# Kernel tuning notes

Measured on AMD Instinct MI355X. Metric: run time of the kernel, lower is better.

## Reference

```python
import jax, jax.numpy as jnp
from jax import lax
import numpy as np

B, T, D_IN = 4, 1024, 8
D_MODEL, N_LAYERS, HORIZON, D_OUT = 512, 2, 24, 8
D_STATE, D_CONV, EXPAND = 64, 4, 2
D_INNER = EXPAND * D_MODEL
DT_RANK = -(-D_MODEL // 16)  # ceil(d_model/16) = 32
LN_EPS = 1e-5


def setup_inputs() -> dict:
    key = jax.random.key(0)
    ks = iter(jax.random.split(key, 24))
    rn = lambda shape, s: jax.random.normal(next(ks), shape, jnp.float32) * s
    A_log = jnp.tile(jnp.log(jnp.arange(1, D_STATE + 1, dtype=jnp.float32)), (N_LAYERS, D_INNER, 1))
    return {
        "x": rn((B, T, D_IN), 1.0),
        "W_in": rn((D_IN, D_MODEL), 0.3), "b_in": jnp.zeros((D_MODEL,), jnp.float32),
        "W_xz": rn((N_LAYERS, D_MODEL, 2 * D_INNER), 0.04),
        "conv_w": rn((N_LAYERS, D_INNER, D_CONV), 0.3), "conv_b": jnp.zeros((N_LAYERS, D_INNER), jnp.float32),
        "W_xproj": rn((N_LAYERS, D_INNER, DT_RANK + 2 * D_STATE), 0.03),
        "W_dt": rn((N_LAYERS, DT_RANK, D_INNER), 0.1), "b_dt": rn((N_LAYERS, D_INNER), 0.1) - 4.0,
        "A_log": A_log, "D_skip": jnp.ones((N_LAYERS, D_INNER), jnp.float32),
        "W_out": rn((N_LAYERS, D_INNER, D_MODEL), 0.03),
        "ln_g": jnp.ones((D_MODEL,), jnp.float32), "ln_b": jnp.zeros((D_MODEL,), jnp.float32),
        "W_h1": rn((D_MODEL, D_MODEL), 0.04), "b_h1": jnp.zeros((D_MODEL,), jnp.float32),
        "W_h2": rn((D_MODEL, HORIZON * D_OUT), 0.04), "b_h2": jnp.zeros((HORIZON * D_OUT,), jnp.float32),
    }


def mamba_block(h, Wxz, cw, cb, Wxp, Wdt, bdt, Alog, Dsk, Wout):
    # h: [B,T,d_model] -> [B,T,d_model]  (mamba-ssm Mamba block, no residual)
    xz = h @ Wxz                                   # [B,T,2*d_inner]
    xb, z = jnp.split(xz, 2, axis=-1)
    # depthwise causal conv over time
    xc = jnp.transpose(xb, (0, 2, 1))              # [B,d_inner,T]
    xc = lax.conv_general_dilated(xc, cw[:, None, :], (1,), [(D_CONV - 1, 0)],
                                  feature_group_count=D_INNER)
    xc = jax.nn.silu(xc + cb[None, :, None])
    xc = jnp.transpose(xc, (0, 2, 1))              # [B,T,d_inner]
    # input-dependent dt, B, C
    xdb = xc @ Wxp                                 # [B,T,dt_rank+2*d_state]
    dt_r = xdb[..., :DT_RANK]
    Bc = xdb[..., DT_RANK:DT_RANK + D_STATE]
    Cc = xdb[..., DT_RANK + D_STATE:]
    dt = jax.nn.softplus(dt_r @ Wdt + bdt)         # [B,T,d_inner]
    A = -jnp.exp(Alog)                             # [d_inner,d_state]

    def step(hst, ins):
        dt_t, B_t, C_t, x_t = ins                  # [B,d_inner],[B,N],[B,N],[B,d_inner]
        dA = jnp.exp(dt_t[..., None] * A)          # [B,d_inner,N]
        hst = dA * hst + dt_t[..., None] * B_t[:, None, :] * x_t[..., None]
        y = jnp.einsum('bdn,bn->bd', hst, C_t)
        return hst, y

    h0 = jnp.zeros((h.shape[0], D_INNER, D_STATE), h.dtype)
    xs = (jnp.transpose(dt, (1, 0, 2)), jnp.transpose(Bc, (1, 0, 2)),
          jnp.transpose(Cc, (1, 0, 2)), jnp.transpose(xc, (1, 0, 2)))
    _, ys = lax.scan(step, h0, xs)                 # ys: [T,B,d_inner]
    y = jnp.transpose(ys, (1, 0, 2)) + Dsk * xc
    y = y * jax.nn.silu(z)
    return y @ Wout


def reference(x, W_in, b_in, W_xz, conv_w, conv_b, W_xproj, W_dt, b_dt, A_log, D_skip,
              W_out, ln_g, ln_b, W_h1, b_h1, W_h2, b_h2):
    h = x @ W_in + b_in                            # [B,T,d_model]
    for i in range(N_LAYERS):
        h = mamba_block(h, W_xz[i], conv_w[i], conv_b[i], W_xproj[i], W_dt[i],
                        b_dt[i], A_log[i], D_skip[i], W_out[i])
    mu = jnp.mean(h, axis=-1, keepdims=True)
    var = jnp.mean(jnp.square(h - mu), axis=-1, keepdims=True)
    h = (h - mu) * lax.rsqrt(var + LN_EPS) * ln_g + ln_b
    last = h[:, -1, :]                             # [B,d_model]
    hid = jax.nn.gelu(last @ W_h1 + b_h1, approximate=False)
    yhat = hid @ W_h2 + b_h2                       # [B,horizon*d_out]
    return yhat.reshape(x.shape[0], HORIZON, D_OUT)
```

## Files before the change

### kernel.cpp

```cpp
#include <hip/hip_runtime.h>
#include <hip/hip_bf16.h>

static constexpr int kB      = 4;
static constexpr int kT      = 1024;
static constexpr int kDIN    = 8;
static constexpr int kDMODEL = 512;
static constexpr int kNLAYER = 2;
static constexpr int kHOR    = 24;
static constexpr int kDOUT   = 8;
static constexpr int kDSTATE = 64;
static constexpr int kDINNER = 1024;
static constexpr int kDTRANK = 32;
static constexpr int kXPROJ  = 160;
static constexpr int kXPAD   = 256;
static constexpr int kBT     = kB * kT;

typedef __bf16 bf16x8 __attribute__((ext_vector_type(8)));
typedef float  f32x4  __attribute__((ext_vector_type(4)));

__device__ __forceinline__ float silu_f(float x)     { return x / (1.f + __expf(-x)); }
__device__ __forceinline__ float softplus_f(float x) { return (x > 20.f) ? x : log1pf(__expf(x)); }
__device__ __forceinline__ float gelu_f(float x)     { return 0.5f * x * (1.f + erff(x * 0.70710678118654752f)); }

__device__ __forceinline__ void gld_lds16(const void* g, void* l) {
    __builtin_amdgcn_global_load_lds(
        (const __attribute__((address_space(1))) unsigned int*)g,
        (__attribute__((address_space(3))) unsigned int*)l, 16, 0, 0);
}

template<int CTRL>
__device__ __forceinline__ float dpp_mov(float v) {
    return __int_as_float(__builtin_amdgcn_update_dpp(
        0, __float_as_int(v), CTRL, 0xf, 0xf, false));
}

__global__ __launch_bounds__(256) void wtrans_kernel(
    const float* __restrict__ in, int K, int N, int in_lstride,
    __hip_bfloat16* __restrict__ out, int Kpad, int out_lstride)
{
    __shared__ float tile[32][33];
    const int tid = threadIdx.x;
    const int n0 = blockIdx.x * 32;
    const int k0 = blockIdx.y * 32;
    const float* inl = in + (size_t)blockIdx.z * in_lstride;
    __hip_bfloat16* outl = out + (size_t)blockIdx.z * out_lstride;

#pragma unroll
    for (int p = 0; p < 4; ++p) {
        int idx = p * 256 + tid;
        int ki = idx >> 5, ni = idx & 31;
        float v = 0.f;
        if (k0 + ki < K && n0 + ni < N) v = inl[(size_t)(k0 + ki) * N + n0 + ni];
        tile[ki][ni] = v;
    }
    __syncthreads();
#pragma unroll
    for (int p = 0; p < 4; ++p) {
        int idx = p * 256 + tid;
        int ni = idx >> 5, ki = idx & 31;
        outl[(size_t)(n0 + ni) * Kpad + k0 + ki] = __float2bfloat16(tile[ki][ni]);
    }
}

template<int MODE>
__global__ __launch_bounds__(256) void mfma_gemm_bt(
    const __hip_bfloat16* __restrict__ A, int lda,
    const __hip_bfloat16* __restrict__ BT, int ldb,
    const float* __restrict__ bias,
    float* __restrict__ C, int ldc,
    void* __restrict__ C2,
    int K)
{
    __shared__ __align__(16) __hip_bfloat16 sA[128][64];
    __shared__ __align__(16) __hip_bfloat16 sB[128][64];

    const int tid  = threadIdx.x;
    const int lane = tid & 63;
    const int w    = tid >> 6;
    const int wm   = w >> 1, wn = w & 1;
    const int m0   = blockIdx.y * 128;
    const int n0   = blockIdx.x * 128;

    f32x4 acc[4][4] = {};

    const int lrow = lane & 15;
    const int lk   = (lane >> 4) << 3;

    const int grow = tid >> 3;
    const int gcol = (tid & 7) * 8;
    char* ldsA = (char*)&sA[0][0] + w * 1024;
    char* ldsB = (char*)&sB[0][0] + w * 1024;

    for (int k0 = 0; k0 < K; k0 += 64) {
        __syncthreads();
#pragma unroll
        for (int p = 0; p < 4; ++p) {
            gld_lds16(A  + (size_t)(m0 + grow + p * 32) * lda + k0 + gcol, ldsA + p * 4096);
            gld_lds16(BT + (size_t)(n0 + grow + p * 32) * ldb + k0 + gcol, ldsB + p * 4096);
        }
        __syncthreads();
#pragma unroll
        for (int ks = 0; ks < 2; ++ks) {
            bf16x8 af[4], bfr[4];
#pragma unroll
            for (int i = 0; i < 4; ++i) {
                af[i]  = *reinterpret_cast<const bf16x8*>(&sA[wm * 64 + i * 16 + lrow][ks * 32 + lk]);
                bfr[i] = *reinterpret_cast<const bf16x8*>(&sB[wn * 64 + i * 16 + lrow][ks * 32 + lk]);
            }
#pragma unroll
            for (int i = 0; i < 4; ++i)
#pragma unroll
                for (int j = 0; j < 4; ++j)
                    acc[i][j] = __builtin_amdgcn_mfma_f32_16x16x32_bf16(af[i], bfr[j], acc[i][j], 0, 0, 0);
        }
    }

    const int crow = (lane >> 4) * 4;
    const int ccol = lane & 15;
#pragma unroll
    for (int i = 0; i < 4; ++i) {
#pragma unroll
        for (int j = 0; j < 4; ++j) {
#pragma unroll
            for (int r = 0; r < 4; ++r) {
                int row = m0 + wm * 64 + i * 16 + crow + r;
                int col = n0 + wn * 64 + j * 16 + ccol;
                float v = acc[i][j][r];
                if (MODE == 1) {
                    C[(size_t)row * ldc + col] = v;
                    ((__hip_bfloat16*)C2)[(size_t)row * ldc + col] = __float2bfloat16(v);
                } else if (MODE == 2) {
                    C[(size_t)row * ldc + col] = softplus_f(v + bias[col]);
                } else if (MODE == 4) {
                    if (col < kDINNER)
                        ((__hip_bfloat16*)C)[(size_t)row * ldc + col] = __float2bfloat16(v);
                    else
                        ((__hip_bfloat16*)C2)[(size_t)row * ldc + (col - kDINNER)] =
                            __float2bfloat16(silu_f(v));
                } else {
                    if (col < kDTRANK)
                        ((__hip_bfloat16*)C2)[(size_t)row * kXPAD + col] = __float2bfloat16(v);
                    else if (col < kDTRANK + kDSTATE)
                        C[(size_t)row * 128 + (col - kDTRANK) * 2] = v;
                    else if (col < kXPROJ)
                        C[(size_t)row * 128 + (col - kDTRANK - kDSTATE) * 2 + 1] = v;
                }
            }
        }
    }
}

__global__ __launch_bounds__(256) void in_proj_kernel(
    const float* __restrict__ x, const float* __restrict__ W,
    const float* __restrict__ b,
    float* __restrict__ h, __hip_bfloat16* __restrict__ hb)
{
    int idx = blockIdx.x * 256 + threadIdx.x;
    int n4 = (idx & 127) * 4;
    int m  = idx >> 7;
    float4 acc = *reinterpret_cast<const float4*>(b + n4);
    const float* xr = x + m * kDIN;
#pragma unroll
    for (int k = 0; k < kDIN; ++k) {
        float4 wv = *reinterpret_cast<const float4*>(W + k * kDMODEL + n4);
        float xv = xr[k];
        acc.x = fmaf(xv, wv.x, acc.x);
        acc.y = fmaf(xv, wv.y, acc.y);
        acc.z = fmaf(xv, wv.z, acc.z);
        acc.w = fmaf(xv, wv.w, acc.w);
    }
    *reinterpret_cast<float4*>(h + (size_t)m * kDMODEL + n4) = acc;
    __bf16 o4[4] = {(__bf16)acc.x, (__bf16)acc.y, (__bf16)acc.z, (__bf16)acc.w};
    *reinterpret_cast<ushort4*>(hb + (size_t)m * kDMODEL + n4) =
        *reinterpret_cast<ushort4*>(o4);
}

__global__ __launch_bounds__(256) void conv_silu_kernel(
    const __hip_bfloat16* __restrict__ xb,
    const float* __restrict__ cw, const float* __restrict__ cb,
    __hip_bfloat16* __restrict__ xc)
{
    int idx = blockIdx.x * 256 + threadIdx.x;
    int dg  = (idx & 127) * 8;
    int bt  = idx >> 7;
    int t   = bt & (kT - 1);

    float4 wv[8];
#pragma unroll
    for (int k = 0; k < 8; ++k)
        wv[k] = *reinterpret_cast<const float4*>(cw + (dg + k) * 4);

    float acc[8];
#pragma unroll
    for (int k = 0; k < 8; ++k) acc[k] = cb[dg + k];

    const __hip_bfloat16* base = xb + (size_t)bt * kDINNER + dg;
    {
        bf16x8 v = *reinterpret_cast<const bf16x8*>(base);
#pragma unroll
        for (int k = 0; k < 8; ++k) acc[k] = fmaf((float)v[k], wv[k].w, acc[k]);
    }
    if (t >= 1) {
        bf16x8 v = *reinterpret_cast<const bf16x8*>(base - kDINNER);
#pragma unroll
        for (int k = 0; k < 8; ++k) acc[k] = fmaf((float)v[k], wv[k].z, acc[k]);
    }
    if (t >= 2) {
        bf16x8 v = *reinterpret_cast<const bf16x8*>(base - 2 * kDINNER);
#pragma unroll
        for (int k = 0; k < 8; ++k) acc[k] = fmaf((float)v[k], wv[k].y, acc[k]);
    }
    if (t >= 3) {
        bf16x8 v = *reinterpret_cast<const bf16x8*>(base - 3 * kDINNER);
#pragma unroll
        for (int k = 0; k < 8; ++k) acc[k] = fmaf((float)v[k], wv[k].x, acc[k]);
    }
    bf16x8 o;
#pragma unroll
    for (int k = 0; k < 8; ++k) o[k] = (__bf16)silu_f(acc[k]);
    *reinterpret_cast<bf16x8*>(xc + (size_t)bt * kDINNER + dg) = o;
}

__global__ __launch_bounds__(256, 4) void scan_kernel(
    const float* __restrict__ dt,
    const float* __restrict__ xdbi,
    const __hip_bfloat16* __restrict__ xc,
    const __hip_bfloat16* __restrict__ zs,
    const float* __restrict__ Alog,
    const float* __restrict__ Dsk,
    __hip_bfloat16* __restrict__ yg)
{
    __shared__ __align__(16) float sBC[2][32][128];
    __shared__ __align__(8)  float sDT[2][32][4][2];

    const int tid  = threadIdx.x;
    const int lane = tid & 63;
    const int w    = tid >> 6;
    const int bb = blockIdx.x;
    const int b  = (bb & 7) >> 1;
    const int d0 = ((bb >> 3) + (bb & 1) * 128) * 4;
    const int d  = d0 + w;

    const float a2  = -__expf(Alog[d * kDSTATE + lane]) * 1.44269504f;
    const float dsk = Dsk[d];
    const size_t rowbase = (size_t)b * kT;
    float s = 0.f;

    auto stageBC = [&](int c, int buf) {
        const float* src = xdbi + (rowbase + c * 32 + w * 8 + (lane >> 5)) * 128
                                + (lane & 31) * 4;
#pragma unroll
        for (int p = 0; p < 4; ++p)
            gld_lds16(src + p * 2 * 128, &sBC[buf][w * 8 + p * 2][0]);
    };
    const int sr = (tid & 127) >> 2, sj = tid & 3;
    auto loadDT = [&](int c, float& odt, float& odx) {
        if (tid < 128) {
            size_t g = (rowbase + c * 32 + sr) * kDINNER + d0 + sj;
            odt = dt[g];
            odx = odt * (float)((const __bf16*)xc)[g];
        }
    };
    auto writeDT = [&](int buf, float vdt, float vdx) {
        if (tid < 128) {
            sDT[buf][sr][sj][0] = vdt;
            sDT[buf][sr][sj][1] = vdx;
        }
    };
    auto loadEP = [&](int c, float& oxv, float& ozv) {
        size_t g = (rowbase + c * 32 + (lane & 31)) * kDINNER + d;
        oxv = (float)((const __bf16*)xc)[g];
        ozv = (float)((const __bf16*)zs)[g];
    };

    float pdt = 0.f, pdx = 0.f, exv = 0.f, ezv = 0.f;
    stageBC(0, 0);
    loadDT(0, pdt, pdx);
    loadEP(0, exv, ezv);
    writeDT(0, pdt, pdx);
    __syncthreads();

    for (int c = 0; c < kT / 32; ++c) {
        const int buf = c & 1;
        float ndt = 0.f, ndx = 0.f, nxv = 0.f, nzv = 0.f;
        const bool more = (c + 1 < kT / 32);
        if (more) {
            stageBC(c + 1, buf ^ 1);
            loadDT(c + 1, ndt, ndx);
            loadEP(c + 1, nxv, nzv);
        }

        float yv[32];
#pragma unroll
        for (int i = 0; i < 32; ++i) {
            float2 bc = *reinterpret_cast<const float2*>(&sBC[buf][i][lane * 2]);
            float2 dd = *reinterpret_cast<const float2*>(&sDT[buf][i][w][0]);
            float dA = exp2f(dd.x * a2);
            s = fmaf(dA, s, dd.y * bc.x);
            yv[i] = s * bc.y;
        }

#pragma unroll
        for (int m = 0; m < 16; ++m) {
            float av = yv[2 * m], bv = yv[2 * m + 1];
            float cv = (lane & 1) ? bv : av;
            float dv = (lane & 1) ? av : bv;
            yv[m] = cv + dpp_mov<0xB1>(dv);
        }
#pragma unroll
        for (int m = 0; m < 8; ++m) {
            float av = yv[2 * m], bv = yv[2 * m + 1];
            float cv = (lane & 2) ? bv : av;
            float dv = (lane & 2) ? av : bv;
            yv[m] = cv + dpp_mov<0x4E>(dv);
        }
#pragma unroll
        for (int j = 2; j < 5; ++j) {
            const int S = 1 << j;
#pragma unroll
            for (int m = 0; m < (32 >> (j + 1)); ++m) {
                float av = yv[2 * m], bv = yv[2 * m + 1];
                float cv = (lane & S) ? bv : av;
                float dv = (lane & S) ? av : bv;
                yv[m] = cv + __shfl_xor(dv, S, 64);
            }
        }
        float y = yv[0];
        y += __shfl_xor(y, 32, 64);

        float yo = fmaf(dsk, exv, y) * ezv;
        if (lane < 32) {
            size_t g = (rowbase + c * 32 + lane) * kDINNER + d;
            yg[g] = __float2bfloat16(yo);
        }
        if (more) writeDT(buf ^ 1, ndt, ndx);
        __syncthreads();
        exv = nxv; ezv = nzv;
    }
}

template<int N, int KK, int ACT>
__global__ __launch_bounds__(256) void head_gemm(
    const float* __restrict__ A,
    const float* __restrict__ B,
    const float* __restrict__ bias,
    float* __restrict__ C)
{
    const int n = blockIdx.x * 64 + (threadIdx.x & 63);
    const int b = threadIdx.x >> 6;
    const float* a  = A + b * KK;
    const float* bp = B + n;
    float acc = 0.f;
#pragma unroll 16
    for (int k = 0; k < KK; ++k)
        acc = fmaf(a[k], bp[(size_t)k * N], acc);
    float v = acc + bias[n];
    if (ACT == 3) v = gelu_f(v);
    C[(size_t)b * N + n] = v;
}

__global__ __launch_bounds__(256) void ln_last_kernel(
    const float* __restrict__ h,
    const float* __restrict__ g, const float* __restrict__ be,
    float* __restrict__ out)
{
    __shared__ float sbuf[8];
    int b = blockIdx.x, tid = threadIdx.x;
    const float* row = h + (size_t)(b * kT + (kT - 1)) * kDMODEL;

    float v0 = row[tid], v1 = row[tid + 256];
    float s = v0 + v1;
    float q = v0 * v0 + v1 * v1;
#pragma unroll
    for (int m = 32; m >= 1; m >>= 1) {
        s += __shfl_xor(s, m, 64);
        q += __shfl_xor(q, m, 64);
    }
    int wid = tid >> 6;
    if ((tid & 63) == 0) { sbuf[wid] = s; sbuf[4 + wid] = q; }
    __syncthreads();
    if (tid == 0) {
        float S = 0.f, Q = 0.f;
        for (int i = 0; i < 4; ++i) { S += sbuf[i]; Q += sbuf[4 + i]; }
        sbuf[0] = S; sbuf[4] = Q;
    }
    __syncthreads();
    float mean = sbuf[0] * (1.f / kDMODEL);
    float var  = sbuf[4] * (1.f / kDMODEL) - mean * mean;
    float inv  = rsqrtf(var + 1e-5f);
    out[b * kDMODEL + tid]       = (v0 - mean) * inv * g[tid]       + be[tid];
    out[b * kDMODEL + tid + 256] = (v1 - mean) * inv * g[tid + 256] + be[tid + 256];
}

extern "C" void kernel_launch(void* const* d_in, const int* in_sizes, int n_in,
                              void* d_out, int out_size, void* d_ws, size_t ws_size,
                              hipStream_t stream)
{
    const float* x      = (const float*)d_in[0];
    const float* W_in   = (const float*)d_in[1];
    const float* b_in   = (const float*)d_in[2];
    const float* W_xz   = (const float*)d_in[3];
    const float* conv_w = (const float*)d_in[4];
    const float* conv_b = (const float*)d_in[5];
    const float* W_xp   = (const float*)d_in[6];
    const float* W_dt   = (const float*)d_in[7];
    const float* b_dt   = (const float*)d_in[8];
    const float* A_log  = (const float*)d_in[9];
    const float* D_skip = (const float*)d_in[10];
    const float* W_out  = (const float*)d_in[11];
    const float* ln_g   = (const float*)d_in[12];
    const float* ln_b   = (const float*)d_in[13];
    const float* W_h1   = (const float*)d_in[14];
    const float* b_h1   = (const float*)d_in[15];
    const float* W_h2   = (const float*)d_in[16];
    const float* b_h2   = (const float*)d_in[17];
    float* out = (float*)d_out;

    char* p = (char*)d_ws;
    auto alloc = [&](size_t bytes) { char* q = p; p += (bytes + 255) & ~(size_t)255; return q; };
    float*          h       = (float*)         alloc((size_t)kBT * kDMODEL * 4);
    __hip_bfloat16* h_bf    = (__hip_bfloat16*)alloc((size_t)kBT * kDMODEL * 2);
    __hip_bfloat16* xb_bf   = (__hip_bfloat16*)alloc((size_t)kBT * kDINNER * 2);
    __hip_bfloat16* z_bf    = (__hip_bfloat16*)alloc((size_t)kBT * kDINNER * 2);
    __hip_bfloat16* xc_bf   = (__hip_bfloat16*)alloc((size_t)kBT * kDINNER * 2);
    float*          xdbi    = (float*)         alloc((size_t)kBT * 128 * 4);
    __hip_bfloat16* xdb_bf  = (__hip_bfloat16*)alloc((size_t)kBT * kXPAD * 2);
    float*          dtb     = (float*)         alloc((size_t)kBT * kDINNER * 4);
    __hip_bfloat16* ys_bf   = (__hip_bfloat16*)alloc((size_t)kBT * kDINNER * 2);
    __hip_bfloat16* wxz_bt  = (__hip_bfloat16*)alloc((size_t)2 * 2048 * 512 * 2);
    __hip_bfloat16* wxp_bt  = (__hip_bfloat16*)alloc((size_t)2 * 256 * 1024 * 2);
    __hip_bfloat16* wdt_bt  = (__hip_bfloat16*)alloc((size_t)2 * 1024 * 64 * 2);
    __hip_bfloat16* wout_bt = (__hip_bfloat16*)alloc((size_t)2 * 512 * 1024 * 2);
    float*          lnb     = (float*)         alloc(kB * kDMODEL * 4);
    float*          hid     = (float*)         alloc(kB * kDMODEL * 4);

    wtrans_kernel<<<dim3(64, 16, 2), 256, 0, stream>>>(W_xz, 512,  2048, 512 * 2048, wxz_bt,  512,  2048 * 512);
    wtrans_kernel<<<dim3(8,  32, 2), 256, 0, stream>>>(W_xp, 1024, 160,  1024 * 160, wxp_bt,  1024, 256 * 1024);
    wtrans_kernel<<<dim3(32, 2,  2), 256, 0, stream>>>(W_dt, 32,   1024, 32 * 1024,  wdt_bt,  64,   1024 * 64);
    wtrans_kernel<<<dim3(16, 32, 2), 256, 0, stream>>>(W_out, 1024, 512, 1024 * 512, wout_bt, 1024, 512 * 1024);

    in_proj_kernel<<<(kBT * 128) / 256, 256, 0, stream>>>(x, W_in, b_in, h, h_bf);

    for (int l = 0; l < kNLAYER; ++l) {
        const float* cw_l  = conv_w + (size_t)l * kDINNER * 4;
        const float* cb_l  = conv_b + (size_t)l * kDINNER;
        const float* bdt_l = b_dt   + (size_t)l * kDINNER;
        const float* Al_l  = A_log  + (size_t)l * kDINNER * kDSTATE;
        const float* Dsk_l = D_skip + (size_t)l * kDINNER;
        const __hip_bfloat16* wxz_l  = wxz_bt  + (size_t)l * 2048 * 512;
        const __hip_bfloat16* wxp_l  = wxp_bt  + (size_t)l * 256 * 1024;
        const __hip_bfloat16* wdt_l  = wdt_bt  + (size_t)l * 1024 * 64;
        const __hip_bfloat16* wout_l = wout_bt + (size_t)l * 512 * 1024;

        mfma_gemm_bt<4><<<dim3(16, 32), 256, 0, stream>>>(
            h_bf, kDMODEL, wxz_l, 512, nullptr, (float*)xb_bf, kDINNER, z_bf, kDMODEL);
        conv_silu_kernel<<<(kBT * 128) / 256, 256, 0, stream>>>(xb_bf, cw_l, cb_l, xc_bf);
        mfma_gemm_bt<5><<<dim3(2, 32), 256, 0, stream>>>(
            xc_bf, kDINNER, wxp_l, 1024, nullptr, xdbi, 128, xdb_bf, kDINNER);
        mfma_gemm_bt<2><<<dim3(8, 32), 256, 0, stream>>>(
            xdb_bf, kXPAD, wdt_l, 64, bdt_l, dtb, kDINNER, nullptr, 64);
        scan_kernel<<<kB * kDINNER / 4, 256, 0, stream>>>(
            dtb, xdbi, xc_bf, z_bf, Al_l, Dsk_l, ys_bf);
        mfma_gemm_bt<1><<<dim3(4, 32), 256, 0, stream>>>(
            ys_bf, kDINNER, wout_l, 1024, nullptr, h, kDMODEL, h_bf, kDINNER);
    }

    ln_last_kernel<<<kB, 256, 0, stream>>>(h, ln_g, ln_b, lnb);
    head_gemm<kDMODEL, kDMODEL, 3><<<kDMODEL / 64, 256, 0, stream>>>(lnb, W_h1, b_h1, hid);
    head_gemm<kHOR * kDOUT, kDMODEL, 0><<<(kHOR * kDOUT) / 64, 256, 0, stream>>>(hid, W_h2, b_h2, out);
}
```

Before: 512.8 us.

## Interleave dt/dx and B/C in time pairs, tile out-proj GEMM narrower, fuse LN+head

The dt GEMM epilogue now computes dt*xc and writes dt and dt*x interleaved in pairs of timesteps, so the scan can stage them into LDS with async loads instead of per-thread global loads. The B/C layout is likewise paired so the scan reads float4 per two steps. The output-projection GEMM gets a 64-wide N tile to launch twice as many blocks. The layernorm and both head GEMMs are fused into one kernel. The main risks are the extra bf16 read in the dt epilogue and a single-block head that runs the W1 loop serially.

```diff
diff --git a/kernel.cpp b/kernel.cpp
--- a/kernel.cpp
+++ b/kernel.cpp
@@ -62,7 +62,7 @@
     }
 }
 
-template<int MODE>
+template<int MODE, int BN>
 __global__ __launch_bounds__(256) void mfma_gemm_bt(
     const __hip_bfloat16* __restrict__ A, int lda,
     const __hip_bfloat16* __restrict__ BT, int ldb,
@@ -72,16 +72,23 @@
     int K)
 {
     __shared__ __align__(16) __hip_bfloat16 sA[128][64];
-    __shared__ __align__(16) __hip_bfloat16 sB[128][64];
+    __shared__ __align__(16) __hip_bfloat16 sB[BN][64];
 
     const int tid  = threadIdx.x;
     const int lane = tid & 63;
     const int w    = tid >> 6;
-    const int wm   = w >> 1, wn = w & 1;
     const int m0   = blockIdx.y * 128;
-    const int n0   = blockIdx.x * 128;
-
-    f32x4 acc[4][4] = {};
+    const int n0   = blockIdx.x * BN;
+
+    constexpr int NI = 4;
+    constexpr int NJ = (BN == 128) ? 4 : 4;
+    constexpr int MI = (BN == 128) ? 4 : 2;
+
+    const int wm = (BN == 128) ? (w >> 1) : w;
+    const int wn = (BN == 128) ? (w & 1) : 0;
+    const int wmrows = (BN == 128) ? 64 : 32;
+
+    f32x4 acc[MI][NJ] = {};
 
     const int lrow = lane & 15;
     const int lk   = (lane >> 4) << 3;
@@ -94,23 +101,25 @@
     for (int k0 = 0; k0 < K; k0 += 64) {
         __syncthreads();
 #pragma unroll
-        for (int p = 0; p < 4; ++p) {
-            gld_lds16(A  + (size_t)(m0 + grow + p * 32) * lda + k0 + gcol, ldsA + p * 4096);
+        for (int p = 0; p < 4; ++p)
+            gld_lds16(A + (size_t)(m0 + grow + p * 32) * lda + k0 + gcol, ldsA + p * 4096);
+#pragma unroll
+        for (int p = 0; p < BN / 32; ++p)
             gld_lds16(BT + (size_t)(n0 + grow + p * 32) * ldb + k0 + gcol, ldsB + p * 4096);
-        }
         __syncthreads();
 #pragma unroll
         for (int ks = 0; ks < 2; ++ks) {
-            bf16x8 af[4], bfr[4];
-#pragma unroll
-            for (int i = 0; i < 4; ++i) {
-                af[i]  = *reinterpret_cast<const bf16x8*>(&sA[wm * 64 + i * 16 + lrow][ks * 32 + lk]);
-                bfr[i] = *reinterpret_cast<const bf16x8*>(&sB[wn * 64 + i * 16 + lrow][ks * 32 + lk]);
-            }
-#pragma unroll
-            for (int i = 0; i < 4; ++i)
-#pragma unroll
-                for (int j = 0; j < 4; ++j)
+            bf16x8 af[MI], bfr[NJ];
+#pragma unroll
+            for (int i = 0; i < MI; ++i)
+                af[i] = *reinterpret_cast<const bf16x8*>(&sA[wm * wmrows + i * 16 + lrow][ks * 32 + lk]);
+#pragma unroll
+            for (int j = 0; j < NJ; ++j)
+                bfr[j] = *reinterpret_cast<const bf16x8*>(&sB[wn * 64 + j * 16 + lrow][ks * 32 + lk]);
+#pragma unroll
+            for (int i = 0; i < MI; ++i)
+#pragma unroll
+                for (int j = 0; j < NJ; ++j)
                     acc[i][j] = __builtin_amdgcn_mfma_f32_16x16x32_bf16(af[i], bfr[j], acc[i][j], 0, 0, 0);
         }
     }
@@ -118,19 +127,23 @@
     const int crow = (lane >> 4) * 4;
     const int ccol = lane & 15;
 #pragma unroll
-    for (int i = 0; i < 4; ++i) {
-#pragma unroll
-        for (int j = 0; j < 4; ++j) {
+    for (int i = 0; i < MI; ++i) {
+#pragma unroll
+        for (int j = 0; j < NJ; ++j) {
 #pragma unroll
             for (int r = 0; r < 4; ++r) {
-                int row = m0 + wm * 64 + i * 16 + crow + r;
+                int row = m0 + wm * wmrows + i * 16 + crow + r;
                 int col = n0 + wn * 64 + j * 16 + ccol;
                 float v = acc[i][j][r];
                 if (MODE == 1) {
                     C[(size_t)row * ldc + col] = v;
                     ((__hip_bfloat16*)C2)[(size_t)row * ldc + col] = __float2bfloat16(v);
                 } else if (MODE == 2) {
-                    C[(size_t)row * ldc + col] = softplus_f(v + bias[col]);
+                    float dtv = softplus_f(v + bias[col]);
+                    float xcv = __bfloat162float(((const __hip_bfloat16*)C2)[(size_t)row * kDINNER + col]);
+                    size_t base = (size_t)(row >> 1) * 4096 + col * 4 + (row & 1) * 2;
+                    C[base]     = dtv;
+                    C[base + 1] = dtv * xcv;
                 } else if (MODE == 4) {
                     if (col < kDINNER)
                         ((__hip_bfloat16*)C)[(size_t)row * ldc + col] = __float2bfloat16(v);
@@ -141,9 +154,9 @@
                     if (col < kDTRANK)
                         ((__hip_bfloat16*)C2)[(size_t)row * kXPAD + col] = __float2bfloat16(v);
                     else if (col < kDTRANK + kDSTATE)
-                        C[(size_t)row * 128 + (col - kDTRANK) * 2] = v;
+                        C[(size_t)(row >> 1) * 256 + (col - kDTRANK) * 4 + (row & 1) * 2] = v;
                     else if (col < kXPROJ)
-                        C[(size_t)row * 128 + (col - kDTRANK - kDSTATE) * 2 + 1] = v;
+                        C[(size_t)(row >> 1) * 256 + (col - kDTRANK - kDSTATE) * 4 + (row & 1) * 2 + 1] = v;
                 }
             }
         }
@@ -222,7 +235,7 @@
 }
 
 __global__ __launch_bounds__(256, 4) void scan_kernel(
-    const float* __restrict__ dt,
+    const float* __restrict__ dtp,
     const float* __restrict__ xdbi,
     const __hip_bfloat16* __restrict__ xc,
     const __hip_bfloat16* __restrict__ zs,
@@ -230,8 +243,8 @@
     const float* __restrict__ Dsk,
     __hip_bfloat16* __restrict__ yg)
 {
-    __shared__ __align__(16) float sBC[2][32][128];
-    __shared__ __align__(8)  float sDT[2][32][4][2];
+    __shared__ __align__(16) float sBC[2][16][64][4];
+    __shared__ __align__(16) float sDT[2][16][4][4];
 
     const int tid  = threadIdx.x;
     const int lane = tid & 63;
@@ -243,29 +256,20 @@
 
     const float a2  = -__expf(Alog[d * kDSTATE + lane]) * 1.44269504f;
     const float dsk = Dsk[d];
-    const size_t rowbase = (size_t)b * kT;
+    const size_t rowbase  = (size_t)b * kT;
+    const size_t pairbase = (size_t)b * (kT / 2);
     float s = 0.f;
 
     auto stageBC = [&](int c, int buf) {
-        const float* src = xdbi + (rowbase + c * 32 + w * 8 + (lane >> 5)) * 128
-                                + (lane & 31) * 4;
+        const float* src = xdbi + (pairbase + c * 16 + 4 * w) * 256 + lane * 4;
 #pragma unroll
         for (int p = 0; p < 4; ++p)
-            gld_lds16(src + p * 2 * 128, &sBC[buf][w * 8 + p * 2][0]);
+            gld_lds16(src + p * 256, &sBC[buf][4 * w + p][0][0]);
     };
-    const int sr = (tid & 127) >> 2, sj = tid & 3;
-    auto loadDT = [&](int c, float& odt, float& odx) {
-        if (tid < 128) {
-            size_t g = (rowbase + c * 32 + sr) * kDINNER + d0 + sj;
-            odt = dt[g];
-            odx = odt * (float)((const __bf16*)xc)[g];
-        }
-    };
-    auto writeDT = [&](int buf, float vdt, float vdx) {
-        if (tid < 128) {
-            sDT[buf][sr][sj][0] = vdt;
-            sDT[buf][sr][sj][1] = vdx;
-        }
+    auto stageDT = [&](int c, int buf) {
+        if (w == 0)
+            gld_lds16(dtp + (pairbase + c * 16 + (lane >> 2)) * 4096 + (d0 + (lane & 3)) * 4,
+                      &sDT[buf][0][0][0]);
     };
     auto loadEP = [&](int c, float& oxv, float& ozv) {
         size_t g = (rowbase + c * 32 + (lane & 31)) * kDINNER + d;
@@ -273,31 +277,33 @@
         ozv = (float)((const __bf16*)zs)[g];
     };
 
-    float pdt = 0.f, pdx = 0.f, exv = 0.f, ezv = 0.f;
+    float exv = 0.f, ezv = 0.f;
     stageBC(0, 0);
-    loadDT(0, pdt, pdx);
+    stageDT(0, 0);
     loadEP(0, exv, ezv);
-    writeDT(0, pdt, pdx);
     __syncthreads();
 
     for (int c = 0; c < kT / 32; ++c) {
         const int buf = c & 1;
-        float ndt = 0.f, ndx = 0.f, nxv = 0.f, nzv = 0.f;
+        float nxv = 0.f, nzv = 0.f;
         const bool more = (c + 1 < kT / 32);
         if (more) {
             stageBC(c + 1, buf ^ 1);
-            loadDT(c + 1, ndt, ndx);
+            stageDT(c + 1, buf ^ 1);
             loadEP(c + 1, nxv, nzv);
         }
 
         float yv[32];
 #pragma unroll
-        for (int i = 0; i < 32; ++i) {
-            float2 bc = *reinterpret_cast<const float2*>(&sBC[buf][i][lane * 2]);
-            float2 dd = *reinterpret_cast<const float2*>(&sDT[buf][i][w][0]);
-            float dA = exp2f(dd.x * a2);
-            s = fmaf(dA, s, dd.y * bc.x);
-            yv[i] = s * bc.y;
+        for (int p = 0; p < 16; ++p) {
+            float4 bc = *reinterpret_cast<const float4*>(&sBC[buf][p][lane][0]);
+            float4 dd = *reinterpret_cast<const float4*>(&sDT[buf][p][w][0]);
+            float dA0 = exp2f(dd.x * a2);
+            s = fmaf(dA0, s, dd.y * bc.x);
+            yv[2 * p] = s * bc.y;
+            float dA1 = exp2f(dd.z * a2);
+            s = fmaf(dA1, s, dd.w * bc.z);
+            yv[2 * p + 1] = s * bc.w;
         }
 
 #pragma unroll
@@ -333,39 +339,22 @@
             size_t g = (rowbase + c * 32 + lane) * kDINNER + d;
             yg[g] = __float2bfloat16(yo);
         }
-        if (more) writeDT(buf ^ 1, ndt, ndx);
         __syncthreads();
         exv = nxv; ezv = nzv;
     }
 }
 
-template<int N, int KK, int ACT>
-__global__ __launch_bounds__(256) void head_gemm(
-    const float* __restrict__ A,
-    const float* __restrict__ B,
-    const float* __restrict__ bias,
-    float* __restrict__ C)
-{
-    const int n = blockIdx.x * 64 + (threadIdx.x & 63);
-    const int b = threadIdx.x >> 6;
-    const float* a  = A + b * KK;
-    const float* bp = B + n;
-    float acc = 0.f;
-#pragma unroll 16
-    for (int k = 0; k < KK; ++k)
-        acc = fmaf(a[k], bp[(size_t)k * N], acc);
-    float v = acc + bias[n];
-    if (ACT == 3) v = gelu_f(v);
-    C[(size_t)b * N + n] = v;
-}
-
-__global__ __launch_bounds__(256) void ln_last_kernel(
+__global__ __launch_bounds__(256) void ln_head_kernel(
     const float* __restrict__ h,
     const float* __restrict__ g, const float* __restrict__ be,
+    const float* __restrict__ W1, const float* __restrict__ b1,
+    const float* __restrict__ W2, const float* __restrict__ b2,
     float* __restrict__ out)
 {
+    __shared__ float sln[512];
+    __shared__ float shid[512];
     __shared__ float sbuf[8];
-    int b = blockIdx.x, tid = threadIdx.x;
+    const int b = blockIdx.x, tid = threadIdx.x;
     const float* row = h + (size_t)(b * kT + (kT - 1)) * kDMODEL;
 
     float v0 = row[tid], v1 = row[tid + 256];
@@ -388,8 +377,28 @@
     float mean = sbuf[0] * (1.f / kDMODEL);
     float var  = sbuf[4] * (1.f / kDMODEL) - mean * mean;
     float inv  = rsqrtf(var + 1e-5f);
-    out[b * kDMODEL + tid]       = (v0 - mean) * inv * g[tid]       + be[tid];
-    out[b * kDMODEL + tid + 256] = (v1 - mean) * inv * g[tid + 256] + be[tid + 256];
+    sln[tid]       = (v0 - mean) * inv * g[tid]       + be[tid];
+    sln[tid + 256] = (v1 - mean) * inv * g[tid + 256] + be[tid + 256];
+    __syncthreads();
+
+    float a0 = b1[tid], a1 = b1[tid + 256];
+#pragma unroll 8
+    for (int k = 0; k < kDMODEL; ++k) {
+        float lv = sln[k];
+        a0 = fmaf(lv, W1[(size_t)k * kDMODEL + tid],       a0);
+        a1 = fmaf(lv, W1[(size_t)k * kDMODEL + tid + 256], a1);
+    }
+    shid[tid]       = gelu_f(a0);
+    shid[tid + 256] = gelu_f(a1);
+    __syncthreads();
+
+    if (tid < kHOR * kDOUT) {
+        float acc = b2[tid];
+#pragma unroll 8
+        for (int k = 0; k < kDMODEL; ++k)
+            acc = fmaf(shid[k], W2[(size_t)k * (kHOR * kDOUT) + tid], acc);
+        out[b * (kHOR * kDOUT) + tid] = acc;
+    }
 }
 
 extern "C" void kernel_launch(void* const* d_in, const int* in_sizes, int n_in,
@@ -423,16 +432,14 @@
     __hip_bfloat16* xb_bf   = (__hip_bfloat16*)alloc((size_t)kBT * kDINNER * 2);
     __hip_bfloat16* z_bf    = (__hip_bfloat16*)alloc((size_t)kBT * kDINNER * 2);
     __hip_bfloat16* xc_bf   = (__hip_bfloat16*)alloc((size_t)kBT * kDINNER * 2);
-    float*          xdbi    = (float*)         alloc((size_t)kBT * 128 * 4);
+    float*          xdbi    = (float*)         alloc((size_t)(kBT / 2) * 256 * 4);
     __hip_bfloat16* xdb_bf  = (__hip_bfloat16*)alloc((size_t)kBT * kXPAD * 2);
-    float*          dtb     = (float*)         alloc((size_t)kBT * kDINNER * 4);
+    float*          dtp     = (float*)         alloc((size_t)(kBT / 2) * 4096 * 4);
     __hip_bfloat16* ys_bf   = (__hip_bfloat16*)alloc((size_t)kBT * kDINNER * 2);
     __hip_bfloat16* wxz_bt  = (__hip_bfloat16*)alloc((size_t)2 * 2048 * 512 * 2);
     __hip_bfloat16* wxp_bt  = (__hip_bfloat16*)alloc((size_t)2 * 256 * 1024 * 2);
     __hip_bfloat16* wdt_bt  = (__hip_bfloat16*)alloc((size_t)2 * 1024 * 64 * 2);
     __hip_bfloat16* wout_bt = (__hip_bfloat16*)alloc((size_t)2 * 512 * 1024 * 2);
-    float*          lnb     = (float*)         alloc(kB * kDMODEL * 4);
-    float*          hid     = (float*)         alloc(kB * kDMODEL * 4);
 
     wtrans_kernel<<<dim3(64, 16, 2), 256, 0, stream>>>(W_xz, 512,  2048, 512 * 2048, wxz_bt,  512,  2048 * 512);
     wtrans_kernel<<<dim3(8,  32, 2), 256, 0, stream>>>(W_xp, 1024, 160,  1024 * 160, wxp_bt,  1024, 256 * 1024);
@@ -452,20 +459,18 @@
         const __hip_bfloat16* wdt_l  = wdt_bt  + (size_t)l * 1024 * 64;
         const __hip_bfloat16* wout_l = wout_bt + (size_t)l * 512 * 1024;
 
-        mfma_gemm_bt<4><<<dim3(16, 32), 256, 0, stream>>>(
+        mfma_gemm_bt<4, 128><<<dim3(16, 32), 256, 0, stream>>>(
             h_bf, kDMODEL, wxz_l, 512, nullptr, (float*)xb_bf, kDINNER, z_bf, kDMODEL);
         conv_silu_kernel<<<(kBT * 128) / 256, 256, 0, stream>>>(xb_bf, cw_l, cb_l, xc_bf);
-        mfma_gemm_bt<5><<<dim3(2, 32), 256, 0, stream>>>(
-            xc_bf, kDINNER, wxp_l, 1024, nullptr, xdbi, 128, xdb_bf, kDINNER);
-        mfma_gemm_bt<2><<<dim3(8, 32), 256, 0, stream>>>(
-            xdb_bf, kXPAD, wdt_l, 64, bdt_l, dtb, kDINNER, nullptr, 64);
+        mfma_gemm_bt<5, 128><<<dim3(2, 32), 256, 0, stream>>>(
+            xc_bf, kDINNER, wxp_l, 1024, nullptr, xdbi, 0, xdb_bf, kDINNER);
+        mfma_gemm_bt<2, 128><<<dim3(8, 32), 256, 0, stream>>>(
+            xdb_bf, kXPAD, wdt_l, 64, bdt_l, dtp, 0, (void*)xc_bf, 64);
         scan_kernel<<<kB * kDINNER / 4, 256, 0, stream>>>(
-            dtb, xdbi, xc_bf, z_bf, Al_l, Dsk_l, ys_bf);
-        mfma_gemm_bt<1><<<dim3(4, 32), 256, 0, stream>>>(
+            dtp, xdbi, xc_bf, z_bf, Al_l, Dsk_l, ys_bf);
+        mfma_gemm_bt<1, 64><<<dim3(8, 32), 256, 0, stream>>>(
             ys_bf, kDINNER, wout_l, 1024, nullptr, h, kDMODEL, h_bf, kDINNER);
     }
 
-    ln_last_kernel<<<kB, 256, 0, stream>>>(h, ln_g, ln_b, lnb);
-    head_gemm<kDMODEL, kDMODEL, 3><<<kDMODEL / 64, 256, 0, stream>>>(lnb, W_h1, b_h1, hid);
-    head_gemm<kHOR * kDOUT, kDMODEL, 0><<<(kHOR * kDOUT) / 64, 256, 0, stream>>>(hid, W_h2, b_h2, out);
-}
+    ln_head_kernel<<<kB, 256, 0, stream>>>(h, ln_g, ln_b, W_h1, b_h1, W_h2, b_h2, out);
+}
```

Measured after the change: 521.2 us. About the same (+1.6%).
